# Kernel tuning notes

Measured on AMD Instinct MI355X. Metric: run time of the kernel, lower is better.

## Reference

```python
import jax, jax.numpy as jnp
import numpy as np

# module hyperparameters (from init_kwargs)
STRIDE, PAD, DIL = 1, 1, 1
GROUPS, DG = 1, 1
KH, KW = 3, 3
CIN, COUT = 256, 256


def _mdcn_forward(x, offset, mask, weight, bias):
    B, C, H, W = x.shape
    Cout = weight.shape[0]
    K = KH * KW
    Ho = (H + 2 * PAD - (DIL * (KH - 1) + 1)) // STRIDE + 1
    Wo = (W + 2 * PAD - (DIL * (KW - 1) + 1)) // STRIDE + 1
    Cg = C // DG

    # offset channel layout: ((g*K + k)*2 + {0: dy, 1: dx})
    off = offset.reshape(B, DG, KH, KW, 2, Ho, Wo)
    base_y = (jnp.arange(Ho) * STRIDE - PAD)[None, :] + DIL * jnp.arange(KH)[:, None]  # [KH,Ho]
    base_x = (jnp.arange(Wo) * STRIDE - PAD)[None, :] + DIL * jnp.arange(KW)[:, None]  # [KW,Wo]
    sy = base_y[None, None, :, None, :, None].astype(x.dtype) + off[:, :, :, :, 0]  # [B,DG,KH,KW,Ho,Wo]
    sx = base_x[None, None, None, :, None, :].astype(x.dtype) + off[:, :, :, :, 1]

    y0f = jnp.floor(sy); x0f = jnp.floor(sx)
    wy = sy - y0f; wx = sx - x0f
    y0 = y0f.astype(jnp.int32); x0 = x0f.astype(jnp.int32)

    xg = x.reshape(B, DG, Cg, H * W)

    def corner(yc, xc, w):
        valid = (yc >= 0) & (yc < H) & (xc >= 0) & (xc < W)
        idx = jnp.clip(yc, 0, H - 1) * W + jnp.clip(xc, 0, W - 1)  # [B,DG,KH,KW,Ho,Wo]
        v = jnp.take_along_axis(xg, idx.reshape(B, DG, 1, -1), axis=3)  # [B,DG,Cg,K*Ho*Wo]
        v = v.reshape(B, DG, Cg, KH, KW, Ho, Wo)
        return v * (w * valid.astype(x.dtype))[:, :, None]

    val = (corner(y0, x0, (1 - wy) * (1 - wx))
           + corner(y0, x0 + 1, (1 - wy) * wx)
           + corner(y0 + 1, x0, wy * (1 - wx))
           + corner(y0 + 1, x0 + 1, wy * wx))  # [B,DG,Cg,KH,KW,Ho,Wo]

    cols = val * mask.reshape(B, DG, 1, KH, KW, Ho, Wo)
    cols = cols.reshape(B, GROUPS, (C // GROUPS) * K, Ho * Wo)
    wg = weight.reshape(GROUPS, Cout // GROUPS, (C // GROUPS) * K)
    out = jnp.einsum('gok,bgkp->bgop', wg, cols).reshape(B, Cout, Ho, Wo)
    return out + bias[None, :, None, None]


def setup_inputs() -> dict:
    key = jax.random.key(0)
    k1, k2, k3, k4 = jax.random.split(key, 4)
    B, H, W = 4, 64, 64
    x = jax.random.normal(k1, (B, CIN, H, W), dtype=jnp.float32)
    offset = jax.random.normal(k2, (B, 2 * DG * KH * KW, H, W), dtype=jnp.float32)
    mask = jax.random.uniform(k3, (B, DG * KH * KW, H, W), dtype=jnp.float32)
    stdv = 1.0 / np.sqrt(CIN * KH * KW)
    weight = jax.random.uniform(k4, (COUT, CIN // GROUPS, KH, KW), dtype=jnp.float32,
                                minval=-stdv, maxval=stdv)
    bias = jnp.zeros((COUT,), dtype=jnp.float32)
    return {"x": x, "offset": offset, "mask": mask, "weight": weight, "bias": bias}


def reference(x, offset, mask, weight, bias):
    return _mdcn_forward(x, offset, mask, weight, bias)
```

## Files before the change

### kernel.cpp

```cpp
#include <hip/hip_runtime.h>
#include <hip/hip_bf16.h>
#include <stdint.h>

#define KDIM 2304

typedef __bf16 bf16_t;
typedef bf16_t bf16x8 __attribute__((ext_vector_type(8)));
typedef float f32x4 __attribute__((ext_vector_type(4)));
typedef float f32x2 __attribute__((ext_vector_type(2)));

__device__ __forceinline__ float b2f_lo(uint32_t u) {
  union { uint32_t i; float f; } c; c.i = u << 16; return c.f;
}
__device__ __forceinline__ float b2f_hi(uint32_t u) {
  union { uint32_t i; float f; } c; c.i = u & 0xffff0000u; return c.f;
}
__device__ __forceinline__ uint32_t pk_bf16(float a, float b) {
  __hip_bfloat162 h = __float22bfloat162_rn(make_float2(a, b));
  union { __hip_bfloat162 h; uint32_t u; } c; c.h = h; return c.u;
}

__device__ __forceinline__ void g2lds16(const uint16_t* g, uint16_t* l) {
  __builtin_amdgcn_global_load_lds((const __attribute__((address_space(1))) void*)g,
                                   (__attribute__((address_space(3))) void*)l,
                                   16, 0, 0);
}

__global__ __launch_bounds__(256) void k_transpose(const float* __restrict__ x,
                                                   uint16_t* __restrict__ xt) {
  __shared__ float tile[32][33];
  int b = blockIdx.z;
  int c0 = blockIdx.y << 5;
  int s0 = blockIdx.x << 5;
  int tid = threadIdx.x;
  int tx = tid & 31, ty = tid >> 5;
  const float* src = x + ((size_t)(b * 256 + c0)) * 4096 + s0;
#pragma unroll
  for (int i = 0; i < 4; ++i)
    tile[ty + i * 8][tx] = src[(size_t)(ty + i * 8) * 4096 + tx];
  __syncthreads();
  int cg = tid & 7, sp = tid >> 3;
  uint2 o;
  o.x = pk_bf16(tile[cg * 4 + 0][sp], tile[cg * 4 + 1][sp]);
  o.y = pk_bf16(tile[cg * 4 + 2][sp], tile[cg * 4 + 3][sp]);
  *(uint2*)&xt[((size_t)b * 4096 + s0 + sp) * 256 + c0 + cg * 4] = o;
}

__global__ __launch_bounds__(256) void k_wprep(const float* __restrict__ w,
                                               uint16_t* __restrict__ wt) {
  int t = blockIdx.x * 256 + threadIdx.x;
  int cout = t / KDIM;
  int r = t - cout * KDIM;
  int k = r >> 8, c = r & 255;
  wt[t] = (uint16_t)(pk_bf16(w[((size_t)(cout * 256 + c)) * 9 + k], 0.f) & 0xffffu);
}

__global__ __launch_bounds__(256) void k_im2col(const uint16_t* __restrict__ xt,
                                                const float* __restrict__ off,
                                                const float* __restrict__ msk,
                                                uint16_t* __restrict__ cols) {
  __shared__ float s_off[18 * 16];
  __shared__ float s_msk[9 * 16];
  int blk = blockIdx.x;
  int wq = blk & 3;
  int ho = (blk >> 2) & 63;
  int b = blk >> 8;
  int w0 = wq << 4;
  int tid = threadIdx.x;
  if (tid < 18 * 16) {
    int ch = tid >> 4, woi = tid & 15;
    s_off[tid] = off[((size_t)(b * 18 + ch)) * 4096 + ho * 64 + w0 + woi];
  } else if (tid >= 64 && tid < 64 + 9 * 16) {
    int i = tid - 64;
  }
  __syncthreads();
  for (int i = tid; i < 18 * 16; i += 256) {
    int ch = i >> 4, woi = i & 15;
    s_off[i] = off[((size_t)(b * 18 + ch)) * 4096 + ho * 64 + w0 + woi];
  }
  for (int i = tid; i < 9 * 16; i += 256) {
    int ch = i >> 4, woi = i & 15;
    s_msk[i] = msk[((size_t)(b * 9 + ch)) * 4096 + ho * 64 + w0 + woi];
  }
  __syncthreads();
  int wv = tid >> 6, lane = tid & 63;
  int half = lane >> 5, li = lane & 31;
  int c8 = li << 3;
  const uint16_t* base = xt + (size_t)b * 4096 * 256;
  uint16_t* cbase = cols + ((size_t)b * 4096 + (size_t)ho * 64 + w0) * KDIM;
  for (int p = wv; p < 72; p += 4) {
    int s = 2 * p + half;
    int k = s >> 4, woi = s & 15;
    int kh = k / 3, kw = k - kh * 3;
    float dy = s_off[(2 * k) * 16 + woi];
    float dx = s_off[(2 * k + 1) * 16 + woi];
    float mm = s_msk[k * 16 + woi];
    float sy = (float)(ho - 1 + kh) + dy;
    float sx = (float)(w0 + woi - 1 + kw) + dx;
    float fy = floorf(sy), fx = floorf(sx);
    int y0 = (int)fy, x0 = (int)fx;
    float wy = sy - fy, wx = sx - fx;
    f32x2 a0 = {0.f, 0.f}, a1 = {0.f, 0.f}, a2 = {0.f, 0.f}, a3 = {0.f, 0.f};
#pragma unroll
    for (int cy = 0; cy < 2; ++cy) {
#pragma unroll
      for (int cx = 0; cx < 2; ++cx) {
        int y = y0 + cy, x = x0 + cx;
        float w = (cy ? wy : 1.f - wy) * (cx ? wx : 1.f - wx);
        bool v = ((unsigned)y < 64u) && ((unsigned)x < 64u);
        w = v ? w : 0.f;
        int yc = min(max(y, 0), 63), xc = min(max(x, 0), 63);
        const uint4 d = *(const uint4*)(base + (((size_t)yc * 64 + xc) * 256 + c8));
        f32x2 ww = {w, w};
        a0 += ww * f32x2{b2f_lo(d.x), b2f_hi(d.x)};
        a1 += ww * f32x2{b2f_lo(d.y), b2f_hi(d.y)};
        a2 += ww * f32x2{b2f_lo(d.z), b2f_hi(d.z)};
        a3 += ww * f32x2{b2f_lo(d.w), b2f_hi(d.w)};
      }
    }
    f32x2 mm2 = {mm, mm};
    a0 *= mm2; a1 *= mm2; a2 *= mm2; a3 *= mm2;
    uint4 o;
    o.x = pk_bf16(a0.x, a0.y);
    o.y = pk_bf16(a1.x, a1.y);
    o.z = pk_bf16(a2.x, a2.y);
    o.w = pk_bf16(a3.x, a3.y);
    *(uint4*)(cbase + (size_t)woi * KDIM + k * 256 + c8) = o;
  }
}

#define BM 128
#define BN 64
#define BK 32
__global__ __launch_bounds__(256) void k_gemm(const uint16_t* __restrict__ A,
                                              const uint16_t* __restrict__ Bm,
                                              const float* __restrict__ bias,
                                              float* __restrict__ out) {
  __shared__ __align__(16) uint16_t As[BM * BK];
  __shared__ __align__(16) uint16_t Bs[BN * BK];
  int tid = threadIdx.x;
  int lane = tid & 63, wv = tid >> 6;
  int wm = wv >> 1, wn = wv & 1;
  int m0 = blockIdx.y * BM, n0 = blockIdx.x * BN;
  int q = lane >> 4, r = lane & 15;

  f32x4 acc[4][2];
#pragma unroll
  for (int i = 0; i < 4; ++i)
#pragma unroll
    for (int j = 0; j < 2; ++j) acc[i][j] = f32x4{0.f, 0.f, 0.f, 0.f};

  const uint16_t* a0p = A + (size_t)(m0 + (tid >> 2)) * KDIM + (tid & 3) * 8;
  const uint16_t* a1p = A + (size_t)(m0 + 64 + (tid >> 2)) * KDIM + (tid & 3) * 8;
  const uint16_t* b0p = Bm + (size_t)(n0 + (tid >> 2)) * KDIM + (tid & 3) * 8;
  uint16_t* as0 = &As[tid * 8];
  uint16_t* as1 = &As[2048 + tid * 8];
  uint16_t* bs0 = &Bs[tid * 8];

  for (int k0 = 0; k0 < KDIM; k0 += BK) {
    g2lds16(a0p + k0, as0);
    g2lds16(a1p + k0, as1);
    g2lds16(b0p + k0, bs0);
    __syncthreads();
    bf16x8 af[4], bfr[2];
#pragma unroll
    for (int mi = 0; mi < 4; ++mi)
      af[mi] = *(const bf16x8*)&As[(wm * 64 + mi * 16 + r) * BK + q * 8];
#pragma unroll
    for (int ni = 0; ni < 2; ++ni)
      bfr[ni] = *(const bf16x8*)&Bs[(wn * 32 + ni * 16 + r) * BK + q * 8];
#pragma unroll
    for (int mi = 0; mi < 4; ++mi)
#pragma unroll
      for (int ni = 0; ni < 2; ++ni)
        acc[mi][ni] = __builtin_amdgcn_mfma_f32_16x16x32_bf16(af[mi], bfr[ni], acc[mi][ni], 0, 0, 0);
    __syncthreads();
  }

#pragma unroll
  for (int mi = 0; mi < 4; ++mi) {
#pragma unroll
    for (int j = 0; j < 4; ++j) {
      int m = m0 + wm * 64 + mi * 16 + q * 4 + j;
      float bv = bias[m];
#pragma unroll
      for (int ni = 0; ni < 2; ++ni) {
        int n = n0 + wn * 32 + ni * 16 + r;
        int b = n >> 12, p = n & 4095;
        out[((size_t)(b * 256 + m)) * 4096 + p] = acc[mi][ni][j] + bv;
      }
    }
  }
}

extern "C" void kernel_launch(void* const* d_in, const int* in_sizes, int n_in,
                              void* d_out, int out_size, void* d_ws, size_t ws_size,
                              hipStream_t stream) {
  (void)in_sizes; (void)n_in; (void)out_size; (void)ws_size;
  const float* x      = (const float*)d_in[0];
  const float* offset = (const float*)d_in[1];
  const float* mask   = (const float*)d_in[2];
  const float* weight = (const float*)d_in[3];
  const float* bias   = (const float*)d_in[4];
  float* out = (float*)d_out;

  uint8_t* ws = (uint8_t*)d_ws;
  uint16_t* xt   = (uint16_t*)ws;
  uint16_t* wt   = (uint16_t*)(ws + 8388608);
  uint16_t* cols = (uint16_t*)(ws + 9568256);

  k_transpose<<<dim3(128, 8, 4), 256, 0, stream>>>(x, xt);
  k_wprep<<<dim3(2304), 256, 0, stream>>>(weight, wt);
  k_im2col<<<dim3(1024), 256, 0, stream>>>(xt, offset, mask, cols);
  k_gemm<<<dim3(256, 2), 256, 0, stream>>>(wt, cols, bias, out);
}
```

Measured before the change: 141.4 us.

## Merge prep kernels, enlarge GEMM tile, add split-K with reduction pass

The transpose and weight-prep kernels are merged into one launch, and the transpose now uses wider tiles with float4 loads. The GEMM N tile doubles to 128, giving more MFMA work per LDS load. When the workspace is large enough, the K dimension is split four ways and a separate pass adds the partial sums, which restores the block count lost to the bigger tile. Split-K writes and reads three extra full-size fp32 partial buffers, adding considerable memory traffic plus one more launch. A redundant offset load and its barrier in im2col are also removed.

```diff
diff --git a/kernel.cpp b/kernel.cpp
--- a/kernel.cpp
+++ b/kernel.cpp
@@ -3,6 +3,7 @@
 #include <stdint.h>
 
 #define KDIM 2304
+#define OUTN 4194304
 
 typedef __bf16 bf16_t;
 typedef bf16_t bf16x8 __attribute__((ext_vector_type(8)));
@@ -26,33 +27,47 @@
                                    16, 0, 0);
 }
 
-__global__ __launch_bounds__(256) void k_transpose(const float* __restrict__ x,
-                                                   uint16_t* __restrict__ xt) {
-  __shared__ float tile[32][33];
-  int b = blockIdx.z;
-  int c0 = blockIdx.y << 5;
-  int s0 = blockIdx.x << 5;
+__global__ __launch_bounds__(256) void k_prep(const float* __restrict__ x,
+                                              uint16_t* __restrict__ xt,
+                                              const float* __restrict__ w,
+                                              uint16_t* __restrict__ wt) {
   int tid = threadIdx.x;
-  int tx = tid & 31, ty = tid >> 5;
-  const float* src = x + ((size_t)(b * 256 + c0)) * 4096 + s0;
-#pragma unroll
-  for (int i = 0; i < 4; ++i)
-    tile[ty + i * 8][tx] = src[(size_t)(ty + i * 8) * 4096 + tx];
-  __syncthreads();
-  int cg = tid & 7, sp = tid >> 3;
-  uint2 o;
-  o.x = pk_bf16(tile[cg * 4 + 0][sp], tile[cg * 4 + 1][sp]);
-  o.y = pk_bf16(tile[cg * 4 + 2][sp], tile[cg * 4 + 3][sp]);
-  *(uint2*)&xt[((size_t)b * 4096 + s0 + sp) * 256 + c0 + cg * 4] = o;
-}
-
-__global__ __launch_bounds__(256) void k_wprep(const float* __restrict__ w,
-                                               uint16_t* __restrict__ wt) {
-  int t = blockIdx.x * 256 + threadIdx.x;
-  int cout = t / KDIM;
-  int r = t - cout * KDIM;
-  int k = r >> 8, c = r & 255;
-  wt[t] = (uint16_t)(pk_bf16(w[((size_t)(cout * 256 + c)) * 9 + k], 0.f) & 0xffffu);
+  if (blockIdx.x < 2048) {
+    __shared__ float tile[32][65];
+    int b = blockIdx.x >> 9;
+    int cgrp = (blockIdx.x >> 6) & 7;
+    int sgrp = blockIdx.x & 63;
+    int c0 = cgrp << 5, s0 = sgrp << 6;
+#pragma unroll
+    for (int it = 0; it < 2; ++it) {
+      int f = tid + it * 256;
+      int rr = f >> 4, col = (f & 15) << 2;
+      float4 v = *(const float4*)&x[((size_t)(b * 256 + c0 + rr)) * 4096 + s0 + col];
+      tile[rr][col + 0] = v.x;
+      tile[rr][col + 1] = v.y;
+      tile[rr][col + 2] = v.z;
+      tile[rr][col + 3] = v.w;
+    }
+    __syncthreads();
+    int sp = tid >> 2, cg = tid & 3;
+    uint4 o;
+    o.x = pk_bf16(tile[cg * 8 + 0][sp], tile[cg * 8 + 1][sp]);
+    o.y = pk_bf16(tile[cg * 8 + 2][sp], tile[cg * 8 + 3][sp]);
+    o.z = pk_bf16(tile[cg * 8 + 4][sp], tile[cg * 8 + 5][sp]);
+    o.w = pk_bf16(tile[cg * 8 + 6][sp], tile[cg * 8 + 7][sp]);
+    *(uint4*)&xt[((size_t)b * 4096 + s0 + sp) * 256 + c0 + cg * 8] = o;
+  } else {
+    __shared__ float wl[2304];
+    int cout = blockIdx.x - 2048;
+    const float* wrow = w + (size_t)cout * 2304;
+    for (int i = tid; i < 576; i += 256)
+      *(float4*)&wl[i * 4] = *(const float4*)&wrow[i * 4];
+    __syncthreads();
+    uint16_t* wdst = wt + (size_t)cout * KDIM + tid;
+#pragma unroll
+    for (int t = 0; t < 9; ++t)
+      wdst[t * 256] = (uint16_t)(pk_bf16(wl[tid * 9 + t], 0.f) & 0xffffu);
+  }
 }
 
 __global__ __launch_bounds__(256) void k_im2col(const uint16_t* __restrict__ xt,
@@ -67,13 +82,6 @@
   int b = blk >> 8;
   int w0 = wq << 4;
   int tid = threadIdx.x;
-  if (tid < 18 * 16) {
-    int ch = tid >> 4, woi = tid & 15;
-    s_off[tid] = off[((size_t)(b * 18 + ch)) * 4096 + ho * 64 + w0 + woi];
-  } else if (tid >= 64 && tid < 64 + 9 * 16) {
-    int i = tid - 64;
-  }
-  __syncthreads();
   for (int i = tid; i < 18 * 16; i += 256) {
     int ch = i >> 4, woi = i & 15;
     s_off[i] = off[((size_t)(b * 18 + ch)) * 4096 + ho * 64 + w0 + woi];
@@ -130,73 +138,95 @@
 }
 
 #define BM 128
-#define BN 64
+#define BN 128
 #define BK 32
 __global__ __launch_bounds__(256) void k_gemm(const uint16_t* __restrict__ A,
                                               const uint16_t* __restrict__ Bm,
                                               const float* __restrict__ bias,
-                                              float* __restrict__ out) {
+                                              float* __restrict__ out,
+                                              float* __restrict__ part,
+                                              int klen) {
   __shared__ __align__(16) uint16_t As[BM * BK];
   __shared__ __align__(16) uint16_t Bs[BN * BK];
   int tid = threadIdx.x;
   int lane = tid & 63, wv = tid >> 6;
   int wm = wv >> 1, wn = wv & 1;
   int m0 = blockIdx.y * BM, n0 = blockIdx.x * BN;
+  int kz = blockIdx.z;
+  int kbeg = kz * klen, kend = kbeg + klen;
   int q = lane >> 4, r = lane & 15;
 
-  f32x4 acc[4][2];
+  f32x4 acc[4][4];
 #pragma unroll
   for (int i = 0; i < 4; ++i)
 #pragma unroll
-    for (int j = 0; j < 2; ++j) acc[i][j] = f32x4{0.f, 0.f, 0.f, 0.f};
+    for (int j = 0; j < 4; ++j) acc[i][j] = f32x4{0.f, 0.f, 0.f, 0.f};
 
   const uint16_t* a0p = A + (size_t)(m0 + (tid >> 2)) * KDIM + (tid & 3) * 8;
   const uint16_t* a1p = A + (size_t)(m0 + 64 + (tid >> 2)) * KDIM + (tid & 3) * 8;
   const uint16_t* b0p = Bm + (size_t)(n0 + (tid >> 2)) * KDIM + (tid & 3) * 8;
+  const uint16_t* b1p = Bm + (size_t)(n0 + 64 + (tid >> 2)) * KDIM + (tid & 3) * 8;
   uint16_t* as0 = &As[tid * 8];
   uint16_t* as1 = &As[2048 + tid * 8];
   uint16_t* bs0 = &Bs[tid * 8];
-
-  for (int k0 = 0; k0 < KDIM; k0 += BK) {
+  uint16_t* bs1 = &Bs[2048 + tid * 8];
+
+  for (int k0 = kbeg; k0 < kend; k0 += BK) {
     g2lds16(a0p + k0, as0);
     g2lds16(a1p + k0, as1);
     g2lds16(b0p + k0, bs0);
-    __syncthreads();
-    bf16x8 af[4], bfr[2];
+    g2lds16(b1p + k0, bs1);
+    __syncthreads();
+    bf16x8 af[4], bfr[4];
 #pragma unroll
     for (int mi = 0; mi < 4; ++mi)
       af[mi] = *(const bf16x8*)&As[(wm * 64 + mi * 16 + r) * BK + q * 8];
 #pragma unroll
-    for (int ni = 0; ni < 2; ++ni)
-      bfr[ni] = *(const bf16x8*)&Bs[(wn * 32 + ni * 16 + r) * BK + q * 8];
+    for (int ni = 0; ni < 4; ++ni)
+      bfr[ni] = *(const bf16x8*)&Bs[(wn * 64 + ni * 16 + r) * BK + q * 8];
 #pragma unroll
     for (int mi = 0; mi < 4; ++mi)
 #pragma unroll
-      for (int ni = 0; ni < 2; ++ni)
+      for (int ni = 0; ni < 4; ++ni)
         acc[mi][ni] = __builtin_amdgcn_mfma_f32_16x16x32_bf16(af[mi], bfr[ni], acc[mi][ni], 0, 0, 0);
     __syncthreads();
   }
 
+  float* dst = (kz == 0) ? out : (part + (size_t)(kz - 1) * OUTN);
 #pragma unroll
   for (int mi = 0; mi < 4; ++mi) {
 #pragma unroll
     for (int j = 0; j < 4; ++j) {
       int m = m0 + wm * 64 + mi * 16 + q * 4 + j;
-      float bv = bias[m];
-#pragma unroll
-      for (int ni = 0; ni < 2; ++ni) {
-        int n = n0 + wn * 32 + ni * 16 + r;
+      float bv = (kz == 0) ? bias[m] : 0.f;
+#pragma unroll
+      for (int ni = 0; ni < 4; ++ni) {
+        int n = n0 + wn * 64 + ni * 16 + r;
         int b = n >> 12, p = n & 4095;
-        out[((size_t)(b * 256 + m)) * 4096 + p] = acc[mi][ni][j] + bv;
+        dst[((size_t)(b * 256 + m)) * 4096 + p] = acc[mi][ni][j] + bv;
       }
     }
   }
+}
+
+__global__ __launch_bounds__(256) void k_reduce(float* __restrict__ out,
+                                                const float* __restrict__ part) {
+  size_t i = ((size_t)blockIdx.x * 256 + threadIdx.x) * 4;
+  float4 o = *(const float4*)&out[i];
+  float4 a = *(const float4*)&part[i];
+  float4 b = *(const float4*)&part[(size_t)OUTN + i];
+  float4 c = *(const float4*)&part[(size_t)2 * OUTN + i];
+  o.x += a.x + b.x + c.x;
+  o.y += a.y + b.y + c.y;
+  o.z += a.z + b.z + c.z;
+  o.w += a.w + b.w + c.w;
+  *(float4*)&out[i] = o;
 }
 
 extern "C" void kernel_launch(void* const* d_in, const int* in_sizes, int n_in,
                               void* d_out, int out_size, void* d_ws, size_t ws_size,
                               hipStream_t stream) {
-  (void)in_sizes; (void)n_in; (void)out_size; (void)ws_size;
+  (void)in_sizes; (void)n_in; (void)out_size;
   const float* x      = (const float*)d_in[0];
   const float* offset = (const float*)d_in[1];
   const float* mask   = (const float*)d_in[2];
@@ -208,9 +238,15 @@
   uint16_t* xt   = (uint16_t*)ws;
   uint16_t* wt   = (uint16_t*)(ws + 8388608);
   uint16_t* cols = (uint16_t*)(ws + 9568256);
-
-  k_transpose<<<dim3(128, 8, 4), 256, 0, stream>>>(x, xt);
-  k_wprep<<<dim3(2304), 256, 0, stream>>>(weight, wt);
+  float*    part = (float*)(ws + 85065728);
+  const bool split = ws_size >= 135397376ULL;
+
+  k_prep<<<dim3(2304), 256, 0, stream>>>(x, xt, weight, wt);
   k_im2col<<<dim3(1024), 256, 0, stream>>>(xt, offset, mask, cols);
-  k_gemm<<<dim3(256, 2), 256, 0, stream>>>(wt, cols, bias, out);
-}
+  if (split) {
+    k_gemm<<<dim3(128, 2, 4), 256, 0, stream>>>(wt, cols, bias, out, part, KDIM / 4);
+    k_reduce<<<dim3(4096), 256, 0, stream>>>(out, part);
+  } else {
+    k_gemm<<<dim3(128, 2, 1), 256, 0, stream>>>(wt, cols, bias, out, part, KDIM);
+  }
+}
```

Result: slower. 151.2 us (+6.9%).
